# Kernel optimization log

Hardware: AMD Instinct MI355X
Metric: run time of the kernel (lower is better)

Reference implementation:

```python
import jax, jax.numpy as jnp
import numpy as np

D = 768  # feature_dim


def setup_inputs() -> dict:
    key = jax.random.key(0)
    ks = jax.random.split(key, 8)
    B, L = 8, 2048
    vision_features = jax.random.normal(ks[0], (B, L, D), dtype=jnp.float32)
    language_features = jax.random.normal(ks[1], (B, L, D), dtype=jnp.float32)
    s = 1.0 / np.sqrt(D)
    Wv = jax.random.uniform(ks[2], (D, D), jnp.float32, -s, s)
    bv = jax.random.uniform(ks[3], (D,), jnp.float32, -s, s)
    Wl = jax.random.uniform(ks[4], (D, D), jnp.float32, -s, s)
    bl = jax.random.uniform(ks[5], (D,), jnp.float32, -s, s)
    so = 1.0 / np.sqrt(2 * D)
    Wo = jax.random.uniform(ks[6], (D, 2 * D), jnp.float32, -so, so)
    bo = jax.random.uniform(ks[7], (D,), jnp.float32, -so, so)
    return {
        "vision_features": vision_features,
        "language_features": language_features,
        "Wv": Wv, "bv": bv, "Wl": Wl, "bl": bl, "Wo": Wo, "bo": bo,
    }


def reference(vision_features, language_features, Wv, bv, Wl, bl, Wo, bo):
    # linear projections (torch Linear: x @ W^T + b)
    vp = jnp.einsum('bld,ed->ble', vision_features, Wv) + bv      # [B,L,D]
    lp = jnp.einsum('bld,ed->ble', language_features, Wl) + bl    # [B,L,D]
    # unscaled bidirectional attention
    sim = jnp.einsum('bid,bjd->bij', vp, lp)                      # [B,L,L]
    attn = jax.nn.softmax(sim, axis=-1)
    aligned_vision = jnp.einsum('bij,bjd->bid', attn, vp)         # [B,L,D]
    aligned_language = jnp.einsum('bij,bid->bjd', attn, lp)       # attn^T @ lp -> [B,L,D]
    combined = jnp.concatenate([aligned_vision, aligned_language], axis=-1)  # [B,L,2D]
    return jnp.einsum('blc,ec->ble', combined, Wo) + bo           # [B,L,D]
```

## Files before the change

kernel.cpp:

```cpp
#include <hip/hip_runtime.h>
#include <stdint.h>

typedef __attribute__((ext_vector_type(8))) short bf16x8;
typedef __attribute__((ext_vector_type(8))) _Float16 f16x8;
typedef __attribute__((ext_vector_type(4))) float f32x4;

__device__ __forceinline__ float b2f(short h) {
  return __uint_as_float(((unsigned)(unsigned short)h) << 16);
}
__device__ __forceinline__ short f2b(float f) {
  unsigned u = __float_as_uint(f);
  u += 0x7fffu + ((u >> 16) & 1u);
  return (short)(u >> 16);
}
__device__ __forceinline__ short f2h(float f) {
  _Float16 h = (_Float16)f;
  return __builtin_bit_cast(short, h);
}
__device__ __forceinline__ float h2f(short s) {
  return (float)__builtin_bit_cast(_Float16, s);
}

__device__ __forceinline__ int swz(int r) { return (r & 6) << 2; }

__device__ __forceinline__ void glds16(const void* g, void* l) {
  __builtin_amdgcn_global_load_lds(
      (const __attribute__((address_space(1))) void*)g,
      (__attribute__((address_space(3))) void*)l, 16, 0, 0);
}

__device__ __forceinline__ void xcd_decode(int C, int RSX, int RPZ,
                                           int& z, int& rowB, int& colB) {
  int id = blockIdx.x;
  int xcd = id & 7, slot = id >> 3;
  int rs = xcd * RSX + slot / C;
  colB = (slot % C) * 128;
  z = rs / RPZ;
  rowB = (rs % RPZ) * 128;
}

__global__ __launch_bounds__(256) void cvt_kernel(
    const float* __restrict__ S0, short* __restrict__ H0, short* __restrict__ L0,
    const float* __restrict__ S1, short* __restrict__ H1, short* __restrict__ L1,
    const float* __restrict__ S2, short* __restrict__ H2, short* __restrict__ L2,
    int n0, int n1, int n2) {
  int g = blockIdx.x * 256 + threadIdx.x;
  const float* s;
  short* h;
  short* l;
  if (g < n0) {
    s = S0 + (size_t)g * 8;
    h = H0 + (size_t)g * 8;
    l = L0 + (size_t)g * 8;
  } else if (g < n0 + n1) {
    size_t t = (size_t)(g - n0);
    s = S1 + t * 8;
    h = H1 + t * 8;
    l = L1 + t * 8;
  } else {
    size_t t = (size_t)(g - n0 - n1);
    s = S2 + t * 8;
    h = H2 + t * 8;
    l = L2 + t * 8;
  }
  float4 v0 = *reinterpret_cast<const float4*>(s);
  float4 v1 = *reinterpret_cast<const float4*>(s + 4);
  float vv[8] = {v0.x, v0.y, v0.z, v0.w, v1.x, v1.y, v1.z, v1.w};
  bf16x8 th, tl;
#pragma unroll
  for (int j = 0; j < 8; ++j) {
    short hh = f2b(vv[j]);
    th[j] = hh;
    tl[j] = f2b(vv[j] - b2f(hh));
  }
  *reinterpret_cast<bf16x8*>(h) = th;
  *reinterpret_cast<bf16x8*>(l) = tl;
}

__global__ __launch_bounds__(256) void zero_kernel(float* __restrict__ p, int n) {
  int i = blockIdx.x * 256 + threadIdx.x;
  if (i < n) p[i] = 0.f;
}
__global__ __launch_bounds__(256) void recip_kernel(const float* __restrict__ s,
                                                    float* __restrict__ invL, int n) {
  int i = blockIdx.x * 256 + threadIdx.x;
  if (i < n) invL[i] = 1.0f / s[i];
}

template <bool SCALE>
__global__ __launch_bounds__(256) void xpose_kernel(
    const short* __restrict__ src0, const float* __restrict__ invL,
    short* __restrict__ dst0) {
  __shared__ alignas(16) short T[64 * 64];
  int id = blockIdx.x;
  int z = id / 384, r = id % 384;
  int it = r / 12, dt = r % 12;
  int i0 = it * 64, d0 = dt * 64;
  const short* src = src0 + (size_t)z * 2048 * 768;
  const float* Lz = SCALE ? (invL + (size_t)z * 2048) : nullptr;
  int t = threadIdx.x;
#pragma unroll
  for (int q = 0; q < 2; ++q) {
    int v = t * 2 + q;
    int ii = v >> 3, dc = (v & 7) * 8;
    bf16x8 x = *reinterpret_cast<const bf16x8*>(&src[(size_t)(i0 + ii) * 768 + d0 + dc]);
    bf16x8 y;
    if constexpr (SCALE) {
      float s = Lz[i0 + ii];
#pragma unroll
      for (int j = 0; j < 8; ++j) y[j] = f2b(b2f(x[j]) * s);
    } else {
#pragma unroll
      for (int j = 0; j < 8; ++j) y[j] = f2b(h2f(x[j]));
    }
    *reinterpret_cast<bf16x8*>(&T[ii * 64 + (dc ^ ((ii & 7) << 3))]) = y;
  }
  __syncthreads();
  short* dst = dst0 + (size_t)z * 768 * 2048;
#pragma unroll
  for (int q = 0; q < 2; ++q) {
    int v = t * 2 + q;
    int dd = v >> 3, is = (v & 7) * 8;
    bf16x8 y;
#pragma unroll
    for (int s2 = 0; s2 < 8; ++s2) {
      int rr = is + s2;
      y[s2] = T[rr * 64 + (dd ^ ((rr & 7) << 3))];
    }
    *reinterpret_cast<bf16x8*>(&dst[(size_t)(d0 + dd) * 2048 + i0 + is]) = y;
  }
}

__global__ __launch_bounds__(256) void transpose_inplace_kernel(short* __restrict__ P) {
  __shared__ alignas(16) short Ta[64 * 64];
  __shared__ alignas(16) short Tb[64 * 64];
  int id = blockIdx.x;
  int z = id >> 10, r = id & 1023;
  int a = r >> 5, b = r & 31;
  if (a > b) return;
  short* Pz = P + (size_t)z * 2048 * 2048;
  int t = threadIdx.x;
#pragma unroll
  for (int q = 0; q < 2; ++q) {
    int v = t * 2 + q;
    int ii = v >> 3, cc = (v & 7) * 8;
    bf16x8 x = *reinterpret_cast<const bf16x8*>(&Pz[(size_t)(a * 64 + ii) * 2048 + b * 64 + cc]);
    *reinterpret_cast<bf16x8*>(&Ta[ii * 64 + (cc ^ ((ii & 7) << 3))]) = x;
    if (a != b) {
      bf16x8 y = *reinterpret_cast<const bf16x8*>(&Pz[(size_t)(b * 64 + ii) * 2048 + a * 64 + cc]);
      *reinterpret_cast<bf16x8*>(&Tb[ii * 64 + (cc ^ ((ii & 7) << 3))]) = y;
    }
  }
  __syncthreads();
#pragma unroll
  for (int q = 0; q < 2; ++q) {
    int v = t * 2 + q;
    int rr = v >> 3, cs = (v & 7) * 8;
    bf16x8 x, y;
#pragma unroll
    for (int s2 = 0; s2 < 8; ++s2) {
      int rs = cs + s2;
      x[s2] = Ta[rs * 64 + (rr ^ ((rs & 7) << 3))];
      if (a != b) y[s2] = Tb[rs * 64 + (rr ^ ((rs & 7) << 3))];
    }
    *reinterpret_cast<bf16x8*>(&Pz[(size_t)(b * 64 + rr) * 2048 + a * 64 + cs]) = x;
    if (a != b)
      *reinterpret_cast<bf16x8*>(&Pz[(size_t)(a * 64 + rr) * 2048 + b * 64 + cs]) = y;
  }
}

template <int OM>
__global__ __launch_bounds__(256) void projg_kernel(
    const short* __restrict__ Ah, const short* __restrict__ Al,
    const short* __restrict__ Bh, const short* __restrict__ Bl,
    const float* __restrict__ bias,
    short* __restrict__ Ch, short* __restrict__ Cl) {
  __shared__ alignas(16) short AsH[128 * 32];
  __shared__ alignas(16) short AsL[128 * 32];
  __shared__ alignas(16) short BsH[128 * 32];
  __shared__ alignas(16) short BsL[128 * 32];
  const int tid = threadIdx.x;
  int z, rowBase, colBase;
  xcd_decode(6, 16, 128, z, rowBase, colBase);
  (void)z;
  const int lane = tid & 63;
  const int ln = lane & 15;
  const int qd = lane >> 4;
  const int w = tid >> 6;
  const int wr = w >> 1, wc = w & 1;

  f32x4 acc[4][4];
#pragma unroll
  for (int i = 0; i < 4; ++i)
#pragma unroll
    for (int j = 0; j < 4; ++j) acc[i][j] = 0.f;

  for (int kb = 0; kb < 768; kb += 32) {
#pragma unroll
    for (int q = 0; q < 2; ++q) {
      int c = q * 256 + tid;
      int r = c >> 2;
      int k0 = ((c & 3) << 3) ^ swz(r);
      size_t ao = (size_t)(rowBase + r) * 768 + kb + k0;
      size_t bo = (size_t)(colBase + r) * 768 + kb + k0;
      glds16(&Ah[ao], &AsH[c * 8]);
      glds16(&Al[ao], &AsL[c * 8]);
      glds16(&Bh[bo], &BsH[c * 8]);
      glds16(&Bl[bo], &BsL[c * 8]);
    }
    __syncthreads();
    bf16x8 ah[4], bh[4], t[4];
#pragma unroll
    for (int rt = 0; rt < 4; ++rt) {
      int m = wr * 64 + rt * 16 + ln;
      ah[rt] = *reinterpret_cast<const bf16x8*>(&AsH[m * 32 + ((qd * 8) ^ swz(m))]);
    }
#pragma unroll
    for (int ct = 0; ct < 4; ++ct) {
      int n = wc * 64 + ct * 16 + ln;
      bh[ct] = *reinterpret_cast<const bf16x8*>(&BsH[n * 32 + ((qd * 8) ^ swz(n))]);
    }
#pragma unroll
    for (int rt = 0; rt < 4; ++rt)
#pragma unroll
      for (int ct = 0; ct < 4; ++ct)
        acc[rt][ct] = __builtin_amdgcn_mfma_f32_16x16x32_bf16(ah[rt], bh[ct], acc[rt][ct], 0, 0, 0);
#pragma unroll
    for (int rt = 0; rt < 4; ++rt) {
      int m = wr * 64 + rt * 16 + ln;
      t[rt] = *reinterpret_cast<const bf16x8*>(&AsL[m * 32 + ((qd * 8) ^ swz(m))]);
    }
#pragma unroll
    for (int rt = 0; rt < 4; ++rt)
#pragma unroll
      for (int ct = 0; ct < 4; ++ct)
        acc[rt][ct] = __builtin_amdgcn_mfma_f32_16x16x32_bf16(t[rt], bh[ct], acc[rt][ct], 0, 0, 0);
#pragma unroll
    for (int ct = 0; ct < 4; ++ct) {
      int n = wc * 64 + ct * 16 + ln;
      t[ct] = *reinterpret_cast<const bf16x8*>(&BsL[n * 32 + ((qd * 8) ^ swz(n))]);
    }
#pragma unroll
    for (int rt = 0; rt < 4; ++rt)
#pragma unroll
      for (int ct = 0; ct < 4; ++ct)
        acc[rt][ct] = __builtin_amdgcn_mfma_f32_16x16x32_bf16(ah[rt], t[ct], acc[rt][ct], 0, 0, 0);
    __syncthreads();
  }

#pragma unroll
  for (int rt = 0; rt < 4; ++rt) {
    int row0 = rowBase + wr * 64 + rt * 16 + qd * 4;
#pragma unroll
    for (int ct = 0; ct < 4; ++ct) {
      int col = colBase + wc * 64 + ct * 16 + ln;
      float bb = bias[col];
      f32x4 a = acc[rt][ct];
#pragma unroll
      for (int r = 0; r < 4; ++r) {
        float val = a[r] + bb;
        if constexpr (OM == 0) {
          Ch[(size_t)(row0 + r) * 768 + col] = f2h(val);
        } else {
          Ch[(size_t)(row0 + r) * 768 + col] = f2b(val);
          Cl[(size_t)(row0 + r) * 768 + col] = f2h(val);
        }
      }
    }
  }
}

__global__ __launch_bounds__(256) void sim2_kernel(const short* __restrict__ vp,
                                                   const short* __restrict__ lp,
                                                   short* __restrict__ P,
                                                   float* __restrict__ S) {
  __shared__ alignas(16) short As[128 * 32];
  __shared__ alignas(16) short Bs[128 * 32];
  const int tid = threadIdx.x;
  int z, rowBase, colBase;
  xcd_decode(16, 16, 16, z, rowBase, colBase);
  const short* Az = vp + (size_t)z * 2048 * 768;
  const short* Bz = lp + (size_t)z * 2048 * 768;
  const int lane = tid & 63;
  const int ln = lane & 15;
  const int qd = lane >> 4;
  const int w = tid >> 6;
  const int wr = w >> 1, wc = w & 1;

  f32x4 acc[4][4];
#pragma unroll
  for (int i = 0; i < 4; ++i)
#pragma unroll
    for (int j = 0; j < 4; ++j) acc[i][j] = 0.f;

  for (int kb = 0; kb < 768; kb += 32) {
#pragma unroll
    for (int q = 0; q < 2; ++q) {
      int c = q * 256 + tid;
      int r = c >> 2;
      int k0 = ((c & 3) << 3) ^ swz(r);
      glds16(&Az[(size_t)(rowBase + r) * 768 + kb + k0], &As[c * 8]);
      glds16(&Bz[(size_t)(colBase + r) * 768 + kb + k0], &Bs[c * 8]);
    }
    __syncthreads();
    f16x8 af[4], bf[4];
#pragma unroll
    for (int rt = 0; rt < 4; ++rt) {
      int m = wr * 64 + rt * 16 + ln;
      af[rt] = *reinterpret_cast<const f16x8*>(&As[m * 32 + ((qd * 8) ^ swz(m))]);
    }
#pragma unroll
    for (int ct = 0; ct < 4; ++ct) {
      int n = wc * 64 + ct * 16 + ln;
      bf[ct] = *reinterpret_cast<const f16x8*>(&Bs[n * 32 + ((qd * 8) ^ swz(n))]);
    }
#pragma unroll
    for (int rt = 0; rt < 4; ++rt)
#pragma unroll
      for (int ct = 0; ct < 4; ++ct)
        acc[rt][ct] = __builtin_amdgcn_mfma_f32_16x16x32_f16(af[rt], bf[ct], acc[rt][ct], 0, 0, 0);
    __syncthreads();
  }

  short* Pz = P + (size_t)z * 2048 * 2048;
  float* Sz = S + (size_t)z * 2048;
#pragma unroll
  for (int rt = 0; rt < 4; ++rt) {
    int row0 = rowBase + wr * 64 + rt * 16 + qd * 4;
    float rowp[4] = {0.f, 0.f, 0.f, 0.f};
#pragma unroll
    for (int ct = 0; ct < 4; ++ct) {
      int col = colBase + wc * 64 + ct * 16 + ln;
      f32x4 a = acc[rt][ct];
#pragma unroll
      for (int r = 0; r < 4; ++r) {
        short h = f2b(__expf(a[r] - 20.0f));
        Pz[(size_t)(row0 + r) * 2048 + col] = h;
        rowp[r] += b2f(h);
      }
    }
#pragma unroll
    for (int r = 0; r < 4; ++r) {
      float v = rowp[r];
      v += __shfl_xor(v, 1);
      v += __shfl_xor(v, 2);
      v += __shfl_xor(v, 4);
      v += __shfl_xor(v, 8);
      if (ln == 0) atomicAdd(&Sz[row0 + r], v);
    }
  }
}

template <int MODE, bool DUALA>
__global__ __launch_bounds__(256) void gemm_k(const short* __restrict__ A,
                                              const short* __restrict__ A2,
                                              const short* __restrict__ B,
                                              void* __restrict__ C,
                                              const float* __restrict__ bias,
                                              const float* __restrict__ invL,
                                              int C_, int RSX_, int RPZ_,
                                              int K, int ldA, int ldB, int ldC,
                                              long sA, long sB, long sC, long sL) {
  __shared__ alignas(16) short As[128 * 32];
  __shared__ alignas(16) short Bs[128 * 32];
  const int tid = threadIdx.x;
  int z, rowBase, colBase;
  xcd_decode(C_, RSX_, RPZ_, z, rowBase, colBase);
  const short* Az = A + (size_t)z * sA;
  const short* Bz = B + (size_t)z * sB;
  const float* Lz = invL ? (invL + (size_t)z * sL) : nullptr;
  const int lane = tid & 63;
  const int ln = lane & 15;
  const int qd = lane >> 4;
  const int w = tid >> 6;
  const int wr = w >> 1, wc = w & 1;

  f32x4 acc[4][4];
#pragma unroll
  for (int i = 0; i < 4; ++i)
#pragma unroll
    for (int j = 0; j < 4; ++j) acc[i][j] = 0.f;

  for (int kb = 0; kb < K; kb += 32) {
#pragma unroll
    for (int q = 0; q < 2; ++q) {
      int c = q * 256 + tid;
      int r = c >> 2;
      int k0 = ((c & 3) << 3) ^ swz(r);
      int kk = kb + k0;
      const short* src;
      if constexpr (DUALA) {
        src = (kk < 768) ? &Az[(size_t)(rowBase + r) * 768 + kk]
                         : &A2[(size_t)(rowBase + r) * 768 + kk - 768];
      } else {
        src = &Az[(size_t)(rowBase + r) * ldA + kk];
      }
      glds16(src, &As[c * 8]);
      glds16(&Bz[(size_t)(colBase + r) * ldB + kb + k0], &Bs[c * 8]);
    }
    __syncthreads();
    bf16x8 af[4], bfv[4];
#pragma unroll
    for (int rt = 0; rt < 4; ++rt) {
      int m = wr * 64 + rt * 16 + ln;
      af[rt] = *reinterpret_cast<const bf16x8*>(&As[m * 32 + ((qd * 8) ^ swz(m))]);
    }
#pragma unroll
    for (int ct = 0; ct < 4; ++ct) {
      int n = wc * 64 + ct * 16 + ln;
      bfv[ct] = *reinterpret_cast<const bf16x8*>(&Bs[n * 32 + ((qd * 8) ^ swz(n))]);
    }
#pragma unroll
    for (int rt = 0; rt < 4; ++rt)
#pragma unroll
      for (int ct = 0; ct < 4; ++ct)
        acc[rt][ct] =
            __builtin_amdgcn_mfma_f32_16x16x32_bf16(af[rt], bfv[ct], acc[rt][ct], 0, 0, 0);
    __syncthreads();
  }

#pragma unroll
  for (int rt = 0; rt < 4; ++rt) {
    int row0 = rowBase + wr * 64 + rt * 16 + qd * 4;
#pragma unroll
    for (int ct = 0; ct < 4; ++ct) {
      int col = colBase + wc * 64 + ct * 16 + ln;
      f32x4 a = acc[rt][ct];
      if constexpr (MODE == 2) {
        short* Co = (short*)C + (size_t)z * sC;
#pragma unroll
        for (int r = 0; r < 4; ++r)
          Co[(size_t)(row0 + r) * ldC + col] = f2b(a[r] * Lz[row0 + r]);
      } else if constexpr (MODE == 3) {
        short* Co = (short*)C + (size_t)z * sC;
#pragma unroll
        for (int r = 0; r < 4; ++r) Co[(size_t)(row0 + r) * ldC + col] = f2b(a[r]);
      } else {
        float* Co = (float*)C + (size_t)z * sC;
        float bb = bias[col];
#pragma unroll
        for (int r = 0; r < 4; ++r) Co[(size_t)(row0 + r) * ldC + col] = a[r] + bb;
      }
    }
  }
}

extern "C" void kernel_launch(void* const* d_in, const int* in_sizes, int n_in,
                              void* d_out, int out_size, void* d_ws, size_t ws_size,
                              hipStream_t stream) {
  const float* vf = (const float*)d_in[0];
  const float* lf = (const float*)d_in[1];
  const float* Wv = (const float*)d_in[2];
  const float* bv = (const float*)d_in[3];
  const float* Wl = (const float*)d_in[4];
  const float* bl = (const float*)d_in[5];
  const float* Wo = (const float*)d_in[6];
  const float* bo = (const float*)d_in[7];

  constexpr int Bz = 8, L = 2048, D = 768, M = Bz * L, D2 = 2 * D;
  constexpr size_t PLANE = (size_t)M * D;
  constexpr size_t WPLANE = (size_t)D * D;

  char* wp = (char*)d_ws;
  auto alloc = [&](size_t bytes) {
    char* p = wp;
    wp += (bytes + 255) & ~(size_t)255;
    return p;
  };
  short* vp16  = (short*)alloc(PLANE * 2);
  short* P     = (short*)alloc((size_t)Bz * L * L * 2);
  float* invL  = (float*)alloc((size_t)M * 4);
  float* sums  = (float*)alloc((size_t)M * 4);

  size_t need_direct = (size_t)(wp - (char*)d_ws) + 2 * PLANE * 2 + 512;
  bool direct = ws_size >= need_direct;

  short *lp_bf, *lp16;
  if (direct) {
    lp_bf = (short*)alloc(PLANE * 2);
    lp16  = (short*)alloc(PLANE * 2);
  } else {
    lp_bf = (short*)d_out;
    lp16  = lp_bf + PLANE;
  }
  short* lpsT = lp16;
  short* vpT  = lp_bf;
  short* av   = vp16;
  short* al   = lp_bf;
  short* woh = P + 2 * PLANE;
  short* wol = woh + (size_t)D * D2;
  float* out_tmp = direct ? (float*)d_out : (float*)P;

  short* fh  = P;
  short* fl  = P + PLANE;
  short* wvh = P + 2 * PLANE;
  short* wvl = wvh + WPLANE;
  short* wlh = wvl + WPLANE;
  short* wll = wlh + WPLANE;

  constexpr int GF  = (int)(PLANE / 8);
  constexpr int GW  = (int)(WPLANE / 8);
  constexpr int GWO = (int)((size_t)D * D2 / 8);

  zero_kernel<<<dim3(M / 256), 256, 0, stream>>>(sums, M);

  cvt_kernel<<<dim3((GF + 2 * GW) / 256), 256, 0, stream>>>(
      vf, fh, fl, Wv, wvh, wvl, Wl, wlh, wll, GF, GW, GW);

  projg_kernel<0><<<dim3(768), 256, 0, stream>>>(fh, fl, wvh, wvl, bv, vp16, nullptr);

  cvt_kernel<<<dim3(GF / 256), 256, 0, stream>>>(
      lf, fh, fl, nullptr, nullptr, nullptr, nullptr, nullptr, nullptr, GF, 0, 0);

  projg_kernel<1><<<dim3(768), 256, 0, stream>>>(fh, fl, wlh, wll, bl, lp_bf, lp16);

  sim2_kernel<<<dim3(2048), 256, 0, stream>>>(vp16, lp16, P, sums);

  recip_kernel<<<dim3(M / 256), 256, 0, stream>>>(sums, invL, M);

  xpose_kernel<true><<<dim3(3072), 256, 0, stream>>>(lp_bf, invL, lpsT);

  xpose_kernel<false><<<dim3(3072), 256, 0, stream>>>(vp16, nullptr, vpT);

  gemm_k<2, false><<<dim3(768), 256, 0, stream>>>(
      P, nullptr, vpT, av, nullptr, invL, 6, 16, 16, L, L, L, D,
      (long)L * L, (long)D * L, (long)L * D, (long)L);

  transpose_inplace_kernel<<<dim3(8192), 256, 0, stream>>>(P);

  gemm_k<3, false><<<dim3(768), 256, 0, stream>>>(
      P, nullptr, lpsT, al, nullptr, nullptr, 6, 16, 16, L, L, L, D,
      (long)L * L, (long)D * L, (long)L * D, (long)L);

  cvt_kernel<<<dim3(GWO / 256), 256, 0, stream>>>(
      Wo, woh, wol, nullptr, nullptr, nullptr, nullptr, nullptr, nullptr, GWO, 0, 0);

  gemm_k<4, true><<<dim3(768), 256, 0, stream>>>(
      av, al, woh, out_tmp, bo, nullptr, 6, 16, 128, D2, D, D2, D, 0, 0, 0, 0);

  if (!direct)
    hipMemcpyAsync(d_out, out_tmp, (size_t)M * D * 4, hipMemcpyDeviceToDevice, stream);
}
```

Measured before the change: 637.9 us.

## Double-buffer LDS tiles in sim and GEMM kernels to overlap loads with MFMA

Both the similarity kernel and the generic GEMM kernel now use two LDS buffers. The next K-tile is issued via global-to-LDS loads before computing on the current one, with vmcnt waits and raw s_barrier in place of __syncthreads. This is meant to hide global memory latency behind MFMA work. It doubles LDS use per block, which may reduce occupancy, and it relies on hand-written waitcnt counts being correct for this load pattern.

Result: faster. 619.9 us (-2.8%).

```diff
diff --git a/kernel.cpp b/kernel.cpp
--- a/kernel.cpp
+++ b/kernel.cpp
@@ -274,8 +274,8 @@
                                                    const short* __restrict__ lp,
                                                    short* __restrict__ P,
                                                    float* __restrict__ S) {
-  __shared__ alignas(16) short As[128 * 32];
-  __shared__ alignas(16) short Bs[128 * 32];
+  __shared__ alignas(16) short As[2][128 * 32];
+  __shared__ alignas(16) short Bs[2][128 * 32];
   const int tid = threadIdx.x;
   int z, rowBase, colBase;
   xcd_decode(16, 16, 16, z, rowBase, colBase);
@@ -293,33 +293,45 @@
 #pragma unroll
     for (int j = 0; j < 4; ++j) acc[i][j] = 0.f;
 
-  for (int kb = 0; kb < 768; kb += 32) {
+  auto stage = [&](int b, int kb) {
 #pragma unroll
     for (int q = 0; q < 2; ++q) {
       int c = q * 256 + tid;
       int r = c >> 2;
       int k0 = ((c & 3) << 3) ^ swz(r);
-      glds16(&Az[(size_t)(rowBase + r) * 768 + kb + k0], &As[c * 8]);
-      glds16(&Bz[(size_t)(colBase + r) * 768 + kb + k0], &Bs[c * 8]);
-    }
-    __syncthreads();
+      glds16(&Az[(size_t)(rowBase + r) * 768 + kb + k0], &As[b][c * 8]);
+      glds16(&Bz[(size_t)(colBase + r) * 768 + kb + k0], &Bs[b][c * 8]);
+    }
+  };
+
+  stage(0, 0);
+  for (int kt = 0; kt < 24; ++kt) {
+    const int cur = kt & 1;
+    if (kt + 1 < 24) {
+      stage(cur ^ 1, (kt + 1) * 32);
+      asm volatile("s_waitcnt vmcnt(4)" ::: "memory");
+    } else {
+      asm volatile("s_waitcnt vmcnt(0)" ::: "memory");
+    }
+    asm volatile("s_barrier" ::: "memory");
     f16x8 af[4], bf[4];
 #pragma unroll
     for (int rt = 0; rt < 4; ++rt) {
       int m = wr * 64 + rt * 16 + ln;
-      af[rt] = *reinterpret_cast<const f16x8*>(&As[m * 32 + ((qd * 8) ^ swz(m))]);
+      af[rt] = *reinterpret_cast<const f16x8*>(&As[cur][m * 32 + ((qd * 8) ^ swz(m))]);
     }
 #pragma unroll
     for (int ct = 0; ct < 4; ++ct) {
       int n = wc * 64 + ct * 16 + ln;
-      bf[ct] = *reinterpret_cast<const f16x8*>(&Bs[n * 32 + ((qd * 8) ^ swz(n))]);
+      bf[ct] = *reinterpret_cast<const f16x8*>(&Bs[cur][n * 32 + ((qd * 8) ^ swz(n))]);
     }
 #pragma unroll
     for (int rt = 0; rt < 4; ++rt)
 #pragma unroll
       for (int ct = 0; ct < 4; ++ct)
         acc[rt][ct] = __builtin_amdgcn_mfma_f32_16x16x32_f16(af[rt], bf[ct], acc[rt][ct], 0, 0, 0);
-    __syncthreads();
+    asm volatile("s_waitcnt lgkmcnt(0)" ::: "memory");
+    asm volatile("s_barrier" ::: "memory");
   }
 
   short* Pz = P + (size_t)z * 2048 * 2048;
@@ -361,8 +373,8 @@
                                               int C_, int RSX_, int RPZ_,
                                               int K, int ldA, int ldB, int ldC,
                                               long sA, long sB, long sC, long sL) {
-  __shared__ alignas(16) short As[128 * 32];
-  __shared__ alignas(16) short Bs[128 * 32];
+  __shared__ alignas(16) short As[2][128 * 32];
+  __shared__ alignas(16) short Bs[2][128 * 32];
   const int tid = threadIdx.x;
   int z, rowBase, colBase;
   xcd_decode(C_, RSX_, RPZ_, z, rowBase, colBase);
@@ -381,7 +393,7 @@
 #pragma unroll
     for (int j = 0; j < 4; ++j) acc[i][j] = 0.f;
 
-  for (int kb = 0; kb < K; kb += 32) {
+  auto stage = [&](int b, int kb) {
 #pragma unroll
     for (int q = 0; q < 2; ++q) {
       int c = q * 256 + tid;
@@ -395,20 +407,32 @@
       } else {
         src = &Az[(size_t)(rowBase + r) * ldA + kk];
       }
-      glds16(src, &As[c * 8]);
-      glds16(&Bz[(size_t)(colBase + r) * ldB + kb + k0], &Bs[c * 8]);
-    }
-    __syncthreads();
+      glds16(src, &As[b][c * 8]);
+      glds16(&Bz[(size_t)(colBase + r) * ldB + kb + k0], &Bs[b][c * 8]);
+    }
+  };
+
+  const int NT = K >> 5;
+  stage(0, 0);
+  for (int kt = 0; kt < NT; ++kt) {
+    const int cur = kt & 1;
+    if (kt + 1 < NT) {
+      stage(cur ^ 1, (kt + 1) << 5);
+      asm volatile("s_waitcnt vmcnt(4)" ::: "memory");
+    } else {
+      asm volatile("s_waitcnt vmcnt(0)" ::: "memory");
+    }
+    asm volatile("s_barrier" ::: "memory");
     bf16x8 af[4], bfv[4];
 #pragma unroll
     for (int rt = 0; rt < 4; ++rt) {
       int m = wr * 64 + rt * 16 + ln;
-      af[rt] = *reinterpret_cast<const bf16x8*>(&As[m * 32 + ((qd * 8) ^ swz(m))]);
+      af[rt] = *reinterpret_cast<const bf16x8*>(&As[cur][m * 32 + ((qd * 8) ^ swz(m))]);
     }
 #pragma unroll
     for (int ct = 0; ct < 4; ++ct) {
       int n = wc * 64 + ct * 16 + ln;
-      bfv[ct] = *reinterpret_cast<const bf16x8*>(&Bs[n * 32 + ((qd * 8) ^ swz(n))]);
+      bfv[ct] = *reinterpret_cast<const bf16x8*>(&Bs[cur][n * 32 + ((qd * 8) ^ swz(n))]);
     }
 #pragma unroll
     for (int rt = 0; rt < 4; ++rt)
@@ -416,7 +440,8 @@
       for (int ct = 0; ct < 4; ++ct)
         acc[rt][ct] =
             __builtin_amdgcn_mfma_f32_16x16x32_bf16(af[rt], bfv[ct], acc[rt][ct], 0, 0, 0);
-    __syncthreads();
+    asm volatile("s_waitcnt lgkmcnt(0)" ::: "memory");
+    asm volatile("s_barrier" ::: "memory");
   }
 
 #pragma unroll
```
